# Kernel optimization log

Hardware: AMD Instinct MI355X
Metric: run time of the kernel (lower is better)

## Reference

```python
import jax, jax.numpy as jnp
import numpy as np

B, N, D, H, C = 2, 2048, 1024, 16, 3
Dh = D // H


def setup_inputs() -> dict:
    key = jax.random.key(0)
    ks = jax.random.split(key, 6)
    x = jax.random.normal(ks[0], (B, N, D), jnp.float32)
    coords = jax.random.normal(ks[1], (B, N, C), jnp.float32)
    attn_mask = jax.random.normal(ks[2], (N, N), jnp.float32) * 0.1  # additive float bias (2d kind)
    Wqkv = jax.random.normal(ks[3], (D, 3 * D), jnp.float32) / np.sqrt(D)
    bqkv = jax.random.normal(ks[4], (3 * D,), jnp.float32) * 0.01
    rel_weight = jax.random.normal(ks[5], (H, C), jnp.float32) * 0.02
    return {"x": x, "coords": coords, "attn_mask": attn_mask,
            "Wqkv": Wqkv, "bqkv": bqkv, "rel_weight": rel_weight}


def reference(x, coords, attn_mask, Wqkv, bqkv, rel_weight):
    b, n, d = x.shape
    h, dh = rel_weight.shape[0], d // rel_weight.shape[0]
    scale = 1.0 / np.sqrt(float(dh))

    qkv = x @ Wqkv + bqkv                      # [B,N,3D]
    q, k, v = jnp.split(qkv, 3, axis=-1)

    def to_heads(t):
        return t.reshape(b, n, h, dh).transpose(0, 2, 1, 3)  # [B,H,N,Dh]

    qh, kh, vh = to_heads(q), to_heads(k), to_heads(v)

    # scaled dot-product scores (flex_attention applies scale before score_mod)
    scores = jnp.einsum('bhnd,bhmd->bhnm', qh, kh) * scale   # [B,H,N,N]

    # coordinate-derived per-head relative bias: coord_proj[b,h,qi] - coord_proj[b,h,kj]
    coord_proj = jnp.einsum('bnc,hc->bhn', coords.astype(jnp.float32), rel_weight)
    scores = scores + coord_proj[:, :, :, None] - coord_proj[:, :, None, :]

    # additive float mask bias, '2d' kind: shape (N,N) broadcast over B,H
    scores = scores + attn_mask[None, None, :, :]

    attn = jax.nn.softmax(scores, axis=-1)
    out = jnp.einsum('bhnm,bhmd->bhnd', attn, vh)            # [B,H,N,Dh]
    return out.transpose(0, 2, 1, 3).reshape(b, n, d)        # [B,N,D]
```

## Files before the change

### kernel.cpp

```cpp
#include <hip/hip_runtime.h>

typedef _Float16 half8 __attribute__((ext_vector_type(8)));
typedef _Float16 half4 __attribute__((ext_vector_type(4)));
typedef _Float16 half2v __attribute__((ext_vector_type(2)));
typedef float floatx4 __attribute__((ext_vector_type(4)));

#define LOG2E 1.44269504088896f
#define QSCALE 0.18033688011112f

__device__ __forceinline__ void async16(const void* g, void* l) {
    __builtin_amdgcn_global_load_lds(
        (const __attribute__((address_space(1))) unsigned int*)g,
        (__attribute__((address_space(3))) unsigned int*)l, 16, 0, 0);
}
__device__ __forceinline__ half4 pack4(float a, float b, float c, float d) {
    half2v lo = __builtin_bit_cast(half2v, __builtin_amdgcn_cvt_pkrtz(a, b));
    half2v hi = __builtin_bit_cast(half2v, __builtin_amdgcn_cvt_pkrtz(c, d));
    half4 r; r[0] = lo[0]; r[1] = lo[1]; r[2] = hi[0]; r[3] = hi[1];
    return r;
}

__global__ __launch_bounds__(256) void k_prep(
    const float* __restrict__ x, const float* __restrict__ W,
    const float* __restrict__ coords, const float* __restrict__ rw,
    const float* __restrict__ mask,
    _Float16* __restrict__ xh, _Float16* __restrict__ Wt,
    _Float16* __restrict__ esch, _Float16* __restrict__ maskp) {
    __shared__ float smem[4352];
    int bx = blockIdx.x, tid = threadIdx.x;
    if (bx < 2048) {
        int i = bx * 256 + tid;
        const floatx4* xin = (const floatx4*)x;
        floatx4 a = xin[i * 2];
        floatx4 b = xin[i * 2 + 1];
        half8 h;
        h[0] = (_Float16)a[0]; h[1] = (_Float16)a[1]; h[2] = (_Float16)a[2]; h[3] = (_Float16)a[3];
        h[4] = (_Float16)b[0]; h[5] = (_Float16)b[1]; h[6] = (_Float16)b[2]; h[7] = (_Float16)b[3];
        *(half8*)&xh[i * 8] = h;
    } else if (bx < 5120) {
        int b2 = bx - 2048;
        int n0 = (b2 % 96) * 32, k0 = (b2 / 96) * 32;
        int tx = tid & 31, ty = tid >> 5;
        float (*tile)[33] = (float(*)[33])smem;
        #pragma unroll
        for (int r = 0; r < 4; ++r)
            tile[ty + r * 8][tx] = W[(size_t)(k0 + ty + r * 8) * 3072 + n0 + tx];
        __syncthreads();
        #pragma unroll
        for (int r = 0; r < 4; ++r)
            Wt[(size_t)(n0 + ty + r * 8) * 1024 + k0 + tx] = (_Float16)tile[tx][ty + r * 8];
    } else if (bx < 5376) {
        int idx = (bx - 5120) * 256 + tid;
        int bh = idx >> 11, n = idx & 2047;
        int b = bh >> 4, h = bh & 15;
        const float* c = &coords[(b * 2048 + n) * 3];
        const float* w = &rw[h * 3];
        float v = -LOG2E * (c[0] * w[0] + c[1] * w[1] + c[2] * w[2]);
        esch[idx] = (_Float16)__builtin_amdgcn_exp2f(v);
    } else {
        int bid = bx - 5376;
        int qt = bid >> 5, kt = bid & 31;
        int row0 = qt * 64, col0 = kt * 64;
        int lr = tid >> 2, lc = (tid & 3) * 16;
        #pragma unroll
        for (int j = 0; j < 4; ++j)
            *(floatx4*)&smem[lr * 68 + lc + j * 4] =
                *(const floatx4*)&mask[(size_t)(row0 + lr) * 2048 + col0 + lc + j * 4];
        __syncthreads();
        int w = tid >> 6, lane = tid & 63, quad = lane >> 4, l16 = lane & 15;
        half4* outp = (half4*)maskp + (size_t)((qt * 32 + kt) * 4 + w) * 256 + lane;
        #pragma unroll
        for (int t = 0; t < 4; ++t) {
            floatx4 m = *(const floatx4*)&smem[(w * 16 + l16) * 68 + t * 16 + quad * 4];
            outp[t * 64] = pack4(m[0] * LOG2E, m[1] * LOG2E, m[2] * LOG2E, m[3] * LOG2E);
        }
    }
}

__global__ __launch_bounds__(256) void k_gemm(
    const _Float16* __restrict__ Ah, const _Float16* __restrict__ Bt,
    const float* __restrict__ bias, const _Float16* __restrict__ esch,
    _Float16* __restrict__ qh, _Float16* __restrict__ kh, _Float16* __restrict__ vt) {
    __shared__ _Float16 smem[16384];
    int tid = threadIdx.x;
    int w = tid >> 6, lane = tid & 63;
    int quad = lane >> 4, l16 = lane & 15;
    int m0 = blockIdx.y * 128;
    int n0 = blockIdx.x * 128;
    bool QK = n0 < 2048;
    int mq = (w >> 1) * 64, nq = (w & 1) * 64;
    int c0 = n0 + nq;

    int rl4 = lane >> 2;
    int pb4 = lane & 3;
    floatx4 acc[4][4] = {};

    const _Float16* ap[2];
    const _Float16* bp[2];
    #pragma unroll
    for (int j = 0; j < 2; ++j) {
        int row = w * 32 + j * 16 + rl4;
        int lb = pb4 ^ (row & 3) ^ ((row >> 2) & 3);
        ap[j] = Ah + (size_t)(m0 + row) * 1024 + lb * 8;
        bp[j] = Bt + (size_t)(n0 + row) * 1024 + lb * 8;
    }

    #define GSTAGE(buf) {                                      \
        _Float16* As_ = smem + (buf) * 8192;                   \
        _Float16* Bs_ = As_ + 4096;                            \
        async16(ap[0], &As_[(w * 32) * 32]);                   \
        async16(ap[1], &As_[(w * 32 + 16) * 32]);              \
        async16(bp[0], &Bs_[(w * 32) * 32]);                   \
        async16(bp[1], &Bs_[(w * 32 + 16) * 32]);              \
        ap[0] += 32; ap[1] += 32; bp[0] += 32; bp[1] += 32;    \
    }

    #define GBODY(cur, last) {                                                         \
        __syncthreads();                                                               \
        if (!(last)) GSTAGE((cur) ^ 1);                                                \
        const _Float16* As_ = smem + (cur) * 8192;                                     \
        const _Float16* Bs_ = As_ + 4096;                                              \
        half8 af[4], bf[4];                                                            \
        _Pragma("unroll")                                                              \
        for (int s = 0; s < 4; ++s) {                                                  \
            int ra = mq + s * 16 + l16;                                                \
            af[s] = *(const half8*)&As_[ra * 32 +                                      \
                ((quad ^ (ra & 3) ^ ((ra >> 2) & 3)) << 3)];                           \
            int rb = nq + s * 16 + l16;                                                \
            bf[s] = *(const half8*)&Bs_[rb * 32 +                                      \
                ((quad ^ (rb & 3) ^ ((rb >> 2) & 3)) << 3)];                           \
        }                                                                              \
        if (QK) {                                                                      \
            _Pragma("unroll")                                                          \
            for (int ms = 0; ms < 4; ++ms)                                             \
                _Pragma("unroll")                                                      \
                for (int ns = 0; ns < 4; ++ns)                                         \
                    acc[ms][ns] = __builtin_amdgcn_mfma_f32_16x16x32_f16(              \
                        bf[ns], af[ms], acc[ms][ns], 0, 0, 0);                         \
        } else {                                                                       \
            _Pragma("unroll")                                                          \
            for (int ms = 0; ms < 4; ++ms)                                             \
                _Pragma("unroll")                                                      \
                for (int ns = 0; ns < 4; ++ns)                                         \
                    acc[ms][ns] = __builtin_amdgcn_mfma_f32_16x16x32_f16(              \
                        af[ms], bf[ns], acc[ms][ns], 0, 0, 0);                         \
        }                                                                              \
    }

    GSTAGE(0);
    #pragma unroll 1
    for (int kt2 = 0; kt2 < 15; ++kt2) {
        GBODY(0, false);
        GBODY(1, false);
    }
    GBODY(0, false);
    GBODY(1, true);
    #undef GBODY
    #undef GSTAGE

    __syncthreads();

    _Float16* Ls = smem + w * 2304;
    int rl = lane >> 3, pb = lane & 7;
    int b = (m0 + mq) >> 11, nbase = (m0 + mq) & 2047;
    if (QK) {
        float qsc = (c0 < 1024) ? QSCALE : 1.0f;
        int h2 = c0 >> 6;
        _Float16* dst = (h2 < 16 ? qh : kh) + (size_t)(((b << 4) + (h2 & 15)) * 2048) * 64;
        int d0 = pb << 3;
        #pragma unroll
        for (int p = 0; p < 2; ++p) {
            #pragma unroll
            for (int ns = 0; ns < 4; ++ns) {
                floatx4 b4 = *(const floatx4*)&bias[c0 + ns * 16 + quad * 4];
                #pragma unroll
                for (int m2 = 0; m2 < 2; ++m2) {
                    int ms = p * 2 + m2;
                    floatx4 v;
                    #pragma unroll
                    for (int i = 0; i < 4; ++i) v[i] = (acc[ms][ns][i] + b4[i]) * qsc;
                    *(half4*)&Ls[(m2 * 16 + l16) * 72 + ns * 16 + quad * 4] =
                        pack4(v[0], v[1], v[2], v[3]);
                }
            }
            #pragma unroll
            for (int rep = 0; rep < 4; ++rep) {
                int nl = rep * 8 + rl;
                half8 v = *(const half8*)&Ls[nl * 72 + d0];
                *(half8*)&dst[(size_t)(nbase + p * 32 + nl) * 64 + d0] = v;
            }
        }
    } else {
        int h = (c0 - 2048) >> 6;
        _Float16* dst = vt + (size_t)(((b << 4) + h) * 64) * 2048;
        const _Float16* ePtr = esch + (size_t)((b << 4) + h) * 2048 + nbase + quad * 4;
        float ef[4][4];
        #pragma unroll
        for (int ms = 0; ms < 4; ++ms) {
            half4 e4 = *(const half4*)&ePtr[ms * 16];
            #pragma unroll
            for (int i = 0; i < 4; ++i) ef[ms][i] = (float)e4[i];
        }
        int noff = pb << 3;
        #pragma unroll
        for (int p = 0; p < 2; ++p) {
            #pragma unroll
            for (int n2 = 0; n2 < 2; ++n2) {
                int ns = p * 2 + n2;
                float bv = bias[c0 + ns * 16 + l16];
                #pragma unroll
                for (int ms = 0; ms < 4; ++ms) {
                    *(half4*)&Ls[(n2 * 16 + l16) * 72 + ms * 16 + quad * 4] =
                        pack4((acc[ms][ns][0] + bv) * ef[ms][0],
                              (acc[ms][ns][1] + bv) * ef[ms][1],
                              (acc[ms][ns][2] + bv) * ef[ms][2],
                              (acc[ms][ns][3] + bv) * ef[ms][3]);
                }
            }
            #pragma unroll
            for (int rep = 0; rep < 4; ++rep) {
                int cl = rep * 8 + rl;
                half8 v = *(const half8*)&Ls[cl * 72 + noff];
                *(half8*)&dst[(size_t)(p * 32 + cl) * 2048 + nbase + noff] = v;
            }
        }
    }
}

__global__ __launch_bounds__(512) __attribute__((amdgpu_waves_per_eu(4)))
void k_attn(
    const _Float16* __restrict__ qh, const _Float16* __restrict__ kh,
    const _Float16* __restrict__ vt, const _Float16* __restrict__ maskp,
    const _Float16* __restrict__ esch, float* __restrict__ out) {
    __shared__ _Float16 KV[2][2][8192];
    __shared__ _Float16 es[2048];
    int tid = threadIdx.x;
    int w = tid >> 6, lane = tid & 63;
    int g2 = w >> 2, wg = w & 3;
    int quad = lane >> 4, l16 = lane & 15;
    int rl = lane >> 3, pb = lane & 7;
    int bid = blockIdx.x;
    int qt2 = bid & 15, bh = bid >> 4;
    int b = bh >> 4, h = bh & 15;
    int qrow = qt2 * 128 + wg * 32;

    *(half4*)&es[tid * 4] = *(const half4*)&esch[(size_t)bh * 2048 + tid * 4];

    half8 qf[2][2];
    #pragma unroll
    for (int g = 0; g < 2; ++g) {
        const _Float16* qp = &qh[((size_t)bh * 2048 + qrow + g * 16 + l16) * 64];
        qf[g][0] = *(const half8*)&qp[quad * 8];
        qf[g][1] = *(const half8*)&qp[32 + quad * 8];
    }
    floatx4 o0[4] = {}, o1[4] = {};
    floatx4 ol0 = {}, ol1 = {};

    int sw = (pb ^ rl) << 3;
    const _Float16* kp0 = kh + (size_t)bh * 131072 + (size_t)(wg * 16 + rl) * 64 + sw
                             + (size_t)g2 * 65536;
    const _Float16* kp1 = kp0 + 512;
    const _Float16* vp0 = vt + (size_t)bh * 131072 + (size_t)(wg * 16 + rl) * 2048 + sw
                             + (size_t)g2 * 1024;
    const _Float16* vp1 = vp0 + 16384;
    const half4* mp0 = (const half4*)maskp +
        ((size_t)(qt2 * 2 + (wg >> 1)) * 128 + (size_t)g2 * 64 + (wg & 1) * 2) * 256 + lane;
    const half4* mp1 = mp0 + 256;
    int ecur = g2 * 1024 + quad * 4;

    half4 mC0[4], mC1[4];

    #define STAGE(buf) {                                             \
        async16(kp0, &KV[g2][buf][(wg * 16) * 64]);                  \
        async16(kp1, &KV[g2][buf][(wg * 16 + 8) * 64]);              \
        async16(vp0, &KV[g2][buf][4096 + (wg * 16) * 64]);           \
        async16(vp1, &KV[g2][buf][4096 + (wg * 16 + 8) * 64]);       \
        kp0 += 4096; kp1 += 4096; vp0 += 64; vp1 += 64;              \
    }

    #define MPREF() {                                                \
        _Pragma("unroll")                                            \
        for (int t = 0; t < 4; ++t) mC0[t] = mp0[t * 64];            \
        _Pragma("unroll")                                            \
        for (int t = 0; t < 4; ++t) mC1[t] = mp1[t * 64];            \
        mp0 += 1024; mp1 += 1024;                                    \
    }

    #define BODY(cur, last) {                                                          \
        __syncthreads();                                                               \
        if (!(last)) STAGE((cur) ^ 1);                                                 \
        const _Float16* Ksc = &KV[g2][cur][0];                                         \
        const _Float16* Vsc = &KV[g2][cur][4096];                                      \
        half4 pt[2][4];                                                                \
        _Pragma("unroll")                                                              \
        for (int t = 0; t < 4; ++t) {                                                  \
            int r = t * 16 + l16;                                                      \
            half8 k0 = *(const half8*)&Ksc[r * 64 + ((quad ^ (r & 7)) << 3)];          \
            half8 k1 = *(const half8*)&Ksc[r * 64 + (((quad + 4) ^ (r & 7)) << 3)];    \
            {                                                                          \
                half4 ml = mC0[t];                                                     \
                floatx4 z;                                                             \
                z[0] = (float)ml[0]; z[1] = (float)ml[1];                              \
                z[2] = (float)ml[2]; z[3] = (float)ml[3];                              \
                z = __builtin_amdgcn_mfma_f32_16x16x32_f16(k0, qf[0][0], z, 0, 0, 0);  \
                z = __builtin_amdgcn_mfma_f32_16x16x32_f16(k1, qf[0][1], z, 0, 0, 0);  \
                pt[0][t] = pack4(__builtin_amdgcn_exp2f(z[0]),                         \
                                 __builtin_amdgcn_exp2f(z[1]),                         \
                                 __builtin_amdgcn_exp2f(z[2]),                         \
                                 __builtin_amdgcn_exp2f(z[3]));                        \
            }                                                                          \
            {                                                                          \
                half4 ml = mC1[t];                                                     \
                floatx4 z;                                                             \
                z[0] = (float)ml[0]; z[1] = (float)ml[1];                              \
                z[2] = (float)ml[2]; z[3] = (float)ml[3];                              \
                z = __builtin_amdgcn_mfma_f32_16x16x32_f16(k0, qf[1][0], z, 0, 0, 0);  \
                z = __builtin_amdgcn_mfma_f32_16x16x32_f16(k1, qf[1][1], z, 0, 0, 0);  \
                pt[1][t] = pack4(__builtin_amdgcn_exp2f(z[0]),                         \
                                 __builtin_amdgcn_exp2f(z[1]),                         \
                                 __builtin_amdgcn_exp2f(z[2]),                         \
                                 __builtin_amdgcn_exp2f(z[3]));                        \
            }                                                                          \
        }                                                                              \
        if (!(last)) MPREF();                                                          \
        _Pragma("unroll")                                                              \
        for (int t = 0; t < 4; ++t) {                                                  \
            half4 ev = *(const half4*)&es[ecur + t * 16];                              \
            ol0 = __builtin_amdgcn_mfma_f32_16x16x16f16(ev, pt[0][t], ol0, 0, 0, 0);   \
            ol1 = __builtin_amdgcn_mfma_f32_16x16x16f16(ev, pt[1][t], ol1, 0, 0, 0);   \
        }                                                                              \
        ecur += 64;                                                                    \
        _Pragma("unroll")                                                              \
        for (int dt = 0; dt < 4; ++dt) {                                               \
            int rv = dt * 16 + l16;                                                    \
            _Pragma("unroll")                                                          \
            for (int t = 0; t < 4; ++t) {                                              \
                half4 vf = *(const half4*)&Vsc[rv * 64 +                               \
                    (((t * 2 + (quad >> 1)) ^ (rv & 7)) << 3) + ((quad & 1) << 2)];    \
                o0[dt] = __builtin_amdgcn_mfma_f32_16x16x16f16(vf, pt[0][t], o0[dt], 0, 0, 0); \
                o1[dt] = __builtin_amdgcn_mfma_f32_16x16x16f16(vf, pt[1][t], o1[dt], 0, 0, 0); \
            }                                                                          \
        }                                                                              \
    }

    STAGE(0);
    MPREF();
    #pragma unroll 1
    for (int kt2 = 0; kt2 < 7; ++kt2) {
        BODY(0, false);
        BODY(1, false);
    }
    BODY(0, false);
    BODY(1, true);
    #undef BODY
    #undef MPREF
    #undef STAGE

    __syncthreads();
    float* comb = (float*)KV;
    {
        float* dst = comb + ((size_t)w * 17) * 64 + lane;
        if (g2 == 0) {
            #pragma unroll
            for (int dt = 0; dt < 4; ++dt)
                #pragma unroll
                for (int i = 0; i < 4; ++i)
                    dst[(dt * 4 + i) * 64] = o1[dt][i];
            dst[16 * 64] = ol1[0];
        } else {
            #pragma unroll
            for (int dt = 0; dt < 4; ++dt)
                #pragma unroll
                for (int i = 0; i < 4; ++i)
                    dst[(dt * 4 + i) * 64] = o0[dt][i];
            dst[16 * 64] = ol0[0];
        }
    }
    __syncthreads();
    {
        const float* src = comb + ((size_t)(w ^ 4) * 17) * 64 + lane;
        if (g2 == 0) {
            #pragma unroll
            for (int dt = 0; dt < 4; ++dt)
                #pragma unroll
                for (int i = 0; i < 4; ++i)
                    o0[dt][i] += src[(dt * 4 + i) * 64];
            float inv = 1.f / (ol0[0] + src[16 * 64]);
            size_t obase = ((size_t)(b * 2048 + qrow + l16)) * 1024 + h * 64 + quad * 4;
            #pragma unroll
            for (int dt = 0; dt < 4; ++dt) {
                floatx4 r;
                #pragma unroll
                for (int i = 0; i < 4; ++i) r[i] = o0[dt][i] * inv;
                *(floatx4*)&out[obase + dt * 16] = r;
            }
        } else {
            #pragma unroll
            for (int dt = 0; dt < 4; ++dt)
                #pragma unroll
                for (int i = 0; i < 4; ++i)
                    o1[dt][i] += src[(dt * 4 + i) * 64];
            float inv = 1.f / (ol1[0] + src[16 * 64]);
            size_t obase = ((size_t)(b * 2048 + qrow + 16 + l16)) * 1024 + h * 64 + quad * 4;
            #pragma unroll
            for (int dt = 0; dt < 4; ++dt) {
                floatx4 r;
                #pragma unroll
                for (int i = 0; i < 4; ++i) r[i] = o1[dt][i] * inv;
                *(floatx4*)&out[obase + dt * 16] = r;
            }
        }
    }
}

extern "C" void kernel_launch(void* const* d_in, const int* in_sizes, int n_in,
                              void* d_out, int out_size, void* d_ws, size_t ws_size,
                              hipStream_t stream) {
    const float* x      = (const float*)d_in[0];
    const float* coords = (const float*)d_in[1];
    const float* mask   = (const float*)d_in[2];
    const float* Wqkv   = (const float*)d_in[3];
    const float* bqkv   = (const float*)d_in[4];
    const float* rw     = (const float*)d_in[5];
    float* out = (float*)d_out;

    char* ws = (char*)d_ws;
    _Float16* xh    = (_Float16*)(ws);
    _Float16* maskp = (_Float16*)(ws + 8388608);
    _Float16* Wt    = (_Float16*)(ws + 16777216);
    _Float16* qh    = (_Float16*)(ws + 23068672);
    _Float16* kh    = (_Float16*)(ws + 31457280);
    _Float16* vt    = (_Float16*)(ws + 39845888);
    _Float16* esch  = (_Float16*)(ws + 48234496);

    k_prep<<<6400, 256, 0, stream>>>(x, Wqkv, coords, rw, mask, xh, Wt, esch, maskp);
    k_gemm<<<dim3(24, 32), 256, 0, stream>>>(xh, Wt, bqkv, esch, qh, kh, vt);
    k_attn<<<512, 512, 0, stream>>>(qh, kh, vt, maskp, esch, out);
}
```

Baseline: 185.6 us.

## Halve attention block size to 64 query rows and 32-key tiles

The attention kernel shrinks from 512 threads covering 128 query rows to 256 threads covering 64 query rows, launching 1024 blocks instead of 512. Each key/value stage now loads 32 keys per split group instead of 64, so the loop runs twice as many iterations. The V staging layout and swizzle, the mask prefetch strides and the combine pairing are rewritten to match. The goal is more blocks and smaller LDS use to improve occupancy and load balance, at the cost of more barriers per key and less reuse of K/V across query rows.

```diff
diff --git a/kernel.cpp b/kernel.cpp
--- a/kernel.cpp
+++ b/kernel.cpp
@@ -227,24 +227,23 @@
     }
 }
 
-__global__ __launch_bounds__(512) __attribute__((amdgpu_waves_per_eu(4)))
+__global__ __launch_bounds__(256) __attribute__((amdgpu_waves_per_eu(4, 4)))
 void k_attn(
     const _Float16* __restrict__ qh, const _Float16* __restrict__ kh,
     const _Float16* __restrict__ vt, const _Float16* __restrict__ maskp,
     const _Float16* __restrict__ esch, float* __restrict__ out) {
-    __shared__ _Float16 KV[2][2][8192];
+    __shared__ _Float16 KV[2][2][4096];
     __shared__ _Float16 es[2048];
     int tid = threadIdx.x;
     int w = tid >> 6, lane = tid & 63;
-    int g2 = w >> 2, wg = w & 3;
+    int g2 = w >> 1, wq = w & 1;
     int quad = lane >> 4, l16 = lane & 15;
-    int rl = lane >> 3, pb = lane & 7;
     int bid = blockIdx.x;
-    int qt2 = bid & 15, bh = bid >> 4;
+    int qt3 = bid & 31, bh = bid >> 5;
     int b = bh >> 4, h = bh & 15;
-    int qrow = qt2 * 128 + wg * 32;
-
-    *(half4*)&es[tid * 4] = *(const half4*)&esch[(size_t)bh * 2048 + tid * 4];
+    int qrow = qt3 * 64 + wq * 32;
+
+    *(half8*)&es[tid * 8] = *(const half8*)&esch[(size_t)bh * 2048 + tid * 8];
 
     half8 qf[2][2];
     #pragma unroll
@@ -256,44 +255,45 @@
     floatx4 o0[4] = {}, o1[4] = {};
     floatx4 ol0 = {}, ol1 = {};
 
-    int sw = (pb ^ rl) << 3;
-    const _Float16* kp0 = kh + (size_t)bh * 131072 + (size_t)(wg * 16 + rl) * 64 + sw
-                             + (size_t)g2 * 65536;
+    int rl = lane >> 3, pb = lane & 7;
+    int swk = (pb ^ rl) << 3;
+    const _Float16* kp0 = kh + (size_t)bh * 131072
+        + (size_t)(g2 * 1024 + wq * 16 + rl) * 64 + swk;
     const _Float16* kp1 = kp0 + 512;
-    const _Float16* vp0 = vt + (size_t)bh * 131072 + (size_t)(wg * 16 + rl) * 2048 + sw
-                             + (size_t)g2 * 1024;
-    const _Float16* vp1 = vp0 + 16384;
+    int lbs = pb ^ (rl & 7);
+    const _Float16* vp0 = vt + (size_t)bh * 131072
+        + (size_t)(wq * 32 + 2 * rl + (lbs >> 2)) * 2048 + g2 * 1024 + ((lbs & 3) << 3);
+    const _Float16* vp1 = vp0 + 16 * 2048;
     const half4* mp0 = (const half4*)maskp +
-        ((size_t)(qt2 * 2 + (wg >> 1)) * 128 + (size_t)g2 * 64 + (wg & 1) * 2) * 256 + lane;
-    const half4* mp1 = mp0 + 256;
+        ((size_t)(qt3 * 32 + g2 * 16) * 4 + wq * 2 + 0) * 256 + lane;
+    const half4* mp1 = (const half4*)maskp +
+        ((size_t)(qt3 * 32 + g2 * 16) * 4 + wq * 2 + 1) * 256 + lane;
     int ecur = g2 * 1024 + quad * 4;
 
-    half4 mC0[4], mC1[4];
+    half4 mC0[2], mC1[2];
 
     #define STAGE(buf) {                                             \
-        async16(kp0, &KV[g2][buf][(wg * 16) * 64]);                  \
-        async16(kp1, &KV[g2][buf][(wg * 16 + 8) * 64]);              \
-        async16(vp0, &KV[g2][buf][4096 + (wg * 16) * 64]);           \
-        async16(vp1, &KV[g2][buf][4096 + (wg * 16 + 8) * 64]);       \
-        kp0 += 4096; kp1 += 4096; vp0 += 64; vp1 += 64;              \
-    }
-
-    #define MPREF() {                                                \
-        _Pragma("unroll")                                            \
-        for (int t = 0; t < 4; ++t) mC0[t] = mp0[t * 64];            \
-        _Pragma("unroll")                                            \
-        for (int t = 0; t < 4; ++t) mC1[t] = mp1[t * 64];            \
-        mp0 += 1024; mp1 += 1024;                                    \
-    }
-
-    #define BODY(cur, last) {                                                          \
+        async16(kp0, &KV[g2][buf][wq * 1024]);                       \
+        async16(kp1, &KV[g2][buf][wq * 1024 + 512]);                 \
+        async16(vp0, &KV[g2][buf][2048 + wq * 1024]);                \
+        async16(vp1, &KV[g2][buf][2048 + wq * 1024 + 512]);          \
+        kp0 += 2048; kp1 += 2048; vp0 += 32; vp1 += 32;              \
+    }
+
+    #define MPREF(d) {                                               \
+        mC0[0] = mp0[0]; mC0[1] = mp0[64];                           \
+        mC1[0] = mp1[0]; mC1[1] = mp1[64];                           \
+        mp0 += (d); mp1 += (d);                                      \
+    }
+
+    #define BODY(cur, last, md) {                                                      \
         __syncthreads();                                                               \
         if (!(last)) STAGE((cur) ^ 1);                                                 \
         const _Float16* Ksc = &KV[g2][cur][0];                                         \
-        const _Float16* Vsc = &KV[g2][cur][4096];                                      \
-        half4 pt[2][4];                                                                \
+        const _Float16* Vsc = &KV[g2][cur][2048];                                      \
+        half4 pt[2][2];                                                                \
         _Pragma("unroll")                                                              \
-        for (int t = 0; t < 4; ++t) {                                                  \
+        for (int t = 0; t < 2; ++t) {                                                  \
             int r = t * 16 + l16;                                                      \
             half8 k0 = *(const half8*)&Ksc[r * 64 + ((quad ^ (r & 7)) << 3)];          \
             half8 k1 = *(const half8*)&Ksc[r * 64 + (((quad + 4) ^ (r & 7)) << 3)];    \
@@ -322,21 +322,23 @@
                                  __builtin_amdgcn_exp2f(z[3]));                        \
             }                                                                          \
         }                                                                              \
-        if (!(last)) MPREF();                                                          \
+        if (!(last)) MPREF(md);                                                        \
         _Pragma("unroll")                                                              \
-        for (int t = 0; t < 4; ++t) {                                                  \
+        for (int t = 0; t < 2; ++t) {                                                  \
             half4 ev = *(const half4*)&es[ecur + t * 16];                              \
             ol0 = __builtin_amdgcn_mfma_f32_16x16x16f16(ev, pt[0][t], ol0, 0, 0, 0);   \
             ol1 = __builtin_amdgcn_mfma_f32_16x16x16f16(ev, pt[1][t], ol1, 0, 0, 0);   \
         }                                                                              \
-        ecur += 64;                                                                    \
+        ecur += 32;                                                                    \
         _Pragma("unroll")                                                              \
         for (int dt = 0; dt < 4; ++dt) {                                               \
             int rv = dt * 16 + l16;                                                    \
+            int sr = rv >> 1;                                                          \
             _Pragma("unroll")                                                          \
-            for (int t = 0; t < 4; ++t) {                                              \
-                half4 vf = *(const half4*)&Vsc[rv * 64 +                               \
-                    (((t * 2 + (quad >> 1)) ^ (rv & 7)) << 3) + ((quad & 1) << 2)];    \
+            for (int t = 0; t < 2; ++t) {                                              \
+                int lb = ((rv & 1) << 2) | (t << 1) | (quad >> 1);                     \
+                half4 vf = *(const half4*)&Vsc[sr * 64 +                               \
+                    ((lb ^ (sr & 7)) << 3) + ((quad & 1) << 2)];                       \
                 o0[dt] = __builtin_amdgcn_mfma_f32_16x16x16f16(vf, pt[0][t], o0[dt], 0, 0, 0); \
                 o1[dt] = __builtin_amdgcn_mfma_f32_16x16x16f16(vf, pt[1][t], o1[dt], 0, 0, 0); \
             }                                                                          \
@@ -344,14 +346,14 @@
     }
 
     STAGE(0);
-    MPREF();
+    MPREF(128);
     #pragma unroll 1
-    for (int kt2 = 0; kt2 < 7; ++kt2) {
-        BODY(0, false);
-        BODY(1, false);
-    }
-    BODY(0, false);
-    BODY(1, true);
+    for (int kt2 = 0; kt2 < 15; ++kt2) {
+        BODY(0, false, 896);
+        BODY(1, false, 128);
+    }
+    BODY(0, false, 896);
+    BODY(1, true, 0);
     #undef BODY
     #undef MPREF
     #undef STAGE
@@ -378,7 +380,7 @@
     }
     __syncthreads();
     {
-        const float* src = comb + ((size_t)(w ^ 4) * 17) * 64 + lane;
+        const float* src = comb + ((size_t)(w ^ 2) * 17) * 64 + lane;
         if (g2 == 0) {
             #pragma unroll
             for (int dt = 0; dt < 4; ++dt)
@@ -435,5 +437,5 @@
 
     k_prep<<<6400, 256, 0, stream>>>(x, Wqkv, coords, rw, mask, xh, Wt, esch, maskp);
     k_gemm<<<dim3(24, 32), 256, 0, stream>>>(xh, Wt, bqkv, esch, qh, kh, vt);
-    k_attn<<<512, 512, 0, stream>>>(qh, kh, vt, maskp, esch, out);
-}
+    k_attn<<<1024, 256, 0, stream>>>(qh, kh, vt, maskp, esch, out);
+}
```

Result: slower. 191.0 us (+2.9%).
